# Kernel tuning notes

Measured on AMD Instinct MI355X. Metric: run time of the kernel, lower is better.

The kernel has to match this reference:

```python
import jax, jax.numpy as jnp
import numpy as np

NUM_EXPERTS = 64
HIDDEN = 4096
TOP_K = 2
B, S = 4, 4096


def setup_inputs() -> dict:
    key = jax.random.key(0)
    k1, k2 = jax.random.split(key)
    hidden_states = jax.random.normal(k1, (B, S, HIDDEN), dtype=jnp.float32)
    W = jax.random.normal(k2, (NUM_EXPERTS, HIDDEN), dtype=jnp.float32) * 0.02
    return {"hidden_states": hidden_states, "W": W}


def reference(hidden_states, W):
    # router logits: [B, S, E]
    logits = jnp.einsum("bsh,eh->bse", hidden_states, W)
    flat = logits.reshape(-1, NUM_EXPERTS)  # [T, E]
    # top-k routing (z-loss / aux-loss do not change forward values; they only
    # inject gradients via the custom autograd function in the torch original)
    scores, top_indices = jax.lax.top_k(flat, TOP_K)  # [T, K] each
    return (scores.reshape(B, S, TOP_K), top_indices.reshape(B, S, TOP_K))
```

## Files before the change

kernel.cpp:

```cpp
#include <hip/hip_runtime.h>
#include <hip/hip_bf16.h>
#include <math.h>

#define NUM_EXPERTS 64
#define HIDDEN      4096
#define T_TOKENS    16384

using short8 = __attribute__((ext_vector_type(8))) short;
using f32x4  = __attribute__((ext_vector_type(4))) float;

__device__ __forceinline__ unsigned pack_pair(float f0, float f1, unsigned& lopk) {
    __hip_bfloat162 h2 = __float22bfloat162_rn(make_float2(f0, f1));
    unsigned hb; __builtin_memcpy(&hb, &h2, 4);
    float h0 = __builtin_bit_cast(float, hb << 16);
    float h1 = __builtin_bit_cast(float, hb & 0xffff0000u);
    __hip_bfloat162 l2 = __float22bfloat162_rn(make_float2(f0 - h0, f1 - h1));
    unsigned lb; __builtin_memcpy(&lb, &l2, 4);
    lopk = lb;
    return hb;
}
__device__ __forceinline__ void split8(const float4 a, const float4 b, uint4& hi, uint4& lo) {
    hi.x = pack_pair(a.x, a.y, lo.x);
    hi.y = pack_pair(a.z, a.w, lo.y);
    hi.z = pack_pair(b.x, b.y, lo.z);
    hi.w = pack_pair(b.z, b.w, lo.w);
}

#define MFMA(a, b, c) __builtin_amdgcn_mfma_f32_16x16x32_bf16((a), (b), (c), 0, 0, 0)

#define GLOAD16(g_, l_)                                                        \
    __builtin_amdgcn_global_load_lds(                                          \
        (__attribute__((address_space(1))) unsigned*)(void*)(g_),              \
        (__attribute__((address_space(3))) unsigned*)(void*)(l_), 16, 0, 0)

#define WAITVM(n_)  asm volatile("s_waitcnt vmcnt(" #n_ ")" ::: "memory")
#define WAITLG()    asm volatile("s_waitcnt lgkmcnt(0)" ::: "memory")
#define SB()        __builtin_amdgcn_sched_barrier(0)

__global__ __launch_bounds__(256) void w_split_kernel(
    const float* __restrict__ W, unsigned char* __restrict__ ws)
{
    const int j  = blockIdx.x * 256 + threadIdx.x;
    const int l  = j & 63;
    const int nt = (j >> 6) & 3;
    const int t  = j >> 8;
    const int e  = nt * 16 + (l & 15);
    const int k0 = t * 32 + ((l >> 4) & 3) * 8;
    const float* p = W + (size_t)e * HIDDEN + k0;
    float4 w0 = *reinterpret_cast<const float4*>(p);
    float4 w1 = *reinterpret_cast<const float4*>(p + 4);
    uint4 hi, lo;
    split8(w0, w1, hi, lo);
    *reinterpret_cast<uint4*>(ws + (size_t)j * 16)            = hi;
    *reinterpret_cast<uint4*>(ws + 524288 + (size_t)j * 16)   = lo;
}


#define LOAD_W(dst, t_) do {                                                   \
    const unsigned char* pW_ = wsHi + (size_t)(tBase + (t_)) * 4096 + laneOff; \
    _Pragma("unroll")                                                          \
    for (int nt_ = 0; nt_ < 4; ++nt_) {                                        \
        dst[nt_]     = *reinterpret_cast<const uint4*>(pW_ + nt_ * 1024);      \
        dst[nt_ + 4] = *reinterpret_cast<const uint4*>(pW_ + 524288 + nt_ * 1024); \
    } } while (0)

#define STAGE_A8(b_, t_) do {                                                  \
    unsigned char* ld_ = smem + (size_t)w * 32768 + (b_) * 16384;              \
    const float* g0_ = aBase + (size_t)(t_) * 32;                              \
    _Pragma("unroll")                                                          \
    for (int mt_ = 0; mt_ < 8; ++mt_) {                                        \
        const float* g_ = g0_ + (size_t)mt_ * 16 * HIDDEN;                     \
        GLOAD16(g_,     ld_ + mt_ * 2048);                                     \
        GLOAD16(g_ + 4, ld_ + mt_ * 2048 + 1024);                              \
    } } while (0)

#define SUB_READ(q_, ls_, mt0_) do {                                           \
    _Pragma("unroll")                                                          \
    for (int i_ = 0; i_ < 4; ++i_) {                                           \
        q_[i_][0] = *reinterpret_cast<const float4*>((ls_) + (mt0_ + i_) * 2048);        \
        q_[i_][1] = *reinterpret_cast<const float4*>((ls_) + (mt0_ + i_) * 2048 + 1024); \
    } } while (0)

#define SUB_MFMA(q_, mt0_, wb_) do {                                           \
    _Pragma("unroll")                                                          \
    for (int i_ = 0; i_ < 4; ++i_) {                                           \
        uint4 hi_, lo_;                                                        \
        split8(q_[i_][0], q_[i_][1], hi_, lo_);                                \
        short8 ah_ = __builtin_bit_cast(short8, hi_);                          \
        short8 al_ = __builtin_bit_cast(short8, lo_);                          \
        _Pragma("unroll")                                                      \
        for (int nt_ = 0; nt_ < 4; ++nt_) {                                    \
            short8 wh_ = __builtin_bit_cast(short8, wb_[nt_]);                 \
            short8 wl_ = __builtin_bit_cast(short8, wb_[nt_ + 4]);             \
            acc[mt0_ + i_][nt_] = MFMA(ah_, wh_, acc[mt0_ + i_][nt_]);         \
            acc[mt0_ + i_][nt_] = MFMA(ah_, wl_, acc[mt0_ + i_][nt_]);         \
            acc[mt0_ + i_][nt_] = MFMA(al_, wh_, acc[mt0_ + i_][nt_]);         \
        } } } while (0)

#define ITER_BODY(t_, buf_, wCur_, wNxt_) do {                                 \
    SB();                                                                      \
    const unsigned char* ls_ = smem + (size_t)w * 32768 + (buf_) * 16384 + laneOff; \
    float4 qA_[4][2];                                                          \
    SUB_READ(qA_, ls_, 0);                                                     \
    WAITLG(); SB();                                                            \
    if ((t_) + 1 < 16) LOAD_W(wNxt_, (t_) + 1);                                \
    SUB_MFMA(qA_, 0, wCur_);                                                   \
    float4 qB_[4][2];                                                          \
    SUB_READ(qB_, ls_, 4);                                                     \
    WAITLG(); SB();                                                            \
    if ((t_) + 2 < 16) STAGE_A8(buf_, (t_) + 2);                               \
    SUB_MFMA(qB_, 4, wCur_);                                                   \
} while (0)

#define ITER(t_, buf_, wCur_, wNxt_)      do { WAITVM(16); ITER_BODY(t_, buf_, wCur_, wNxt_); } while (0)
#define ITER_LAST(t_, buf_, wCur_, wNxt_) do { WAITVM(0);  ITER_BODY(t_, buf_, wCur_, wNxt_); } while (0)

__global__ __launch_bounds__(256, 1) void router_gemm_partial(
    const float* __restrict__ A,
    const unsigned char* __restrict__ wsHi,
    float* __restrict__ partG)
{
    __shared__ unsigned char smem[131072];

    const int tid  = threadIdx.x;
    const int lane = tid & 63;
    const int w    = tid >> 6;
    const int ky   = blockIdx.y;
    const int tok0 = blockIdx.x * 128;
    const int tBase = ky * 64 + w * 16;

    const float* aBase = A + (size_t)(tok0 + (lane & 15)) * HIDDEN
                           + ky * 2048 + w * 512 + ((lane >> 4) & 3) * 8;
    const int laneOff = lane * 16;

    f32x4 acc[8][4];
#pragma unroll
    for (int mt = 0; mt < 8; ++mt)
#pragma unroll
        for (int nt = 0; nt < 4; ++nt) acc[mt][nt] = (f32x4){0.f, 0.f, 0.f, 0.f};

    uint4 wX[8], wY[8];

    LOAD_W(wX, 0);
    STAGE_A8(0, 0);
    STAGE_A8(1, 1);

    ITER( 0, 0, wX, wY);  ITER( 1, 1, wY, wX);
    ITER( 2, 0, wX, wY);  ITER( 3, 1, wY, wX);
    ITER( 4, 0, wX, wY);  ITER( 5, 1, wY, wX);
    ITER( 6, 0, wX, wY);  ITER( 7, 1, wY, wX);
    ITER( 8, 0, wX, wY);  ITER( 9, 1, wY, wX);
    ITER(10, 0, wX, wY);  ITER(11, 1, wY, wX);
    ITER(12, 0, wX, wY);  ITER(13, 1, wY, wX);
    ITER(14, 0, wX, wY);  ITER_LAST(15, 1, wY, wX);

    f32x4 (*part)[8][4][64] = reinterpret_cast<f32x4 (*)[8][4][64]>(smem);

    __syncthreads();
#pragma unroll
    for (int mt = 0; mt < 8; ++mt)
#pragma unroll
        for (int nt = 0; nt < 4; ++nt) part[w][mt][nt][lane] = acc[mt][nt];
    __syncthreads();

#pragma unroll
    for (int j = 0; j < 2; ++j) {
        const int mt = 2 * w + j;
#pragma unroll
        for (int nt = 0; nt < 4; ++nt) {
            f32x4 s = part[0][mt][nt][lane];
#pragma unroll
            for (int q = 1; q < 4; ++q) s = s + part[q][mt][nt][lane];
            const int e = nt * 16 + (lane & 15);
#pragma unroll
            for (int r = 0; r < 4; ++r) {
                const int tok = tok0 + mt * 16 + (lane >> 4) * 4 + r;
                partG[((size_t)ky * T_TOKENS + tok) * 64 + e] = s[r];
            }
        }
    }
}

__global__ __launch_bounds__(64) void combine_topk(
    const float* __restrict__ partG,
    float* __restrict__ out)
{
    const int tok = blockIdx.x * 64 + threadIdx.x;
    const float4* p0 = reinterpret_cast<const float4*>(partG + (size_t)tok * 64);
    const float4* p1 = reinterpret_cast<const float4*>(partG + ((size_t)T_TOKENS + tok) * 64);

    float s[64];
#pragma unroll
    for (int i = 0; i < 16; ++i) {
        float4 a = p0[i], b = p1[i];
        s[4*i+0] = a.x + b.x; s[4*i+1] = a.y + b.y;
        s[4*i+2] = a.z + b.z; s[4*i+3] = a.w + b.w;
    }

    float b1 = -INFINITY, b2 = -INFINITY;
    int i1 = 0, i2 = 0;
#pragma unroll
    for (int e = 0; e < NUM_EXPERTS; ++e) {
        float v = s[e];
        if (v > b1)      { b2 = b1; i2 = i1; b1 = v; i1 = e; }
        else if (v > b2) { b2 = v;  i2 = e; }
    }
    out[(size_t)tok * 2 + 0] = b1;
    out[(size_t)tok * 2 + 1] = b2;
    out[(size_t)2 * T_TOKENS + (size_t)tok * 2 + 0] = (float)i1;
    out[(size_t)2 * T_TOKENS + (size_t)tok * 2 + 1] = (float)i2;
}

extern "C" void kernel_launch(void* const* d_in, const int* in_sizes, int n_in,
                              void* d_out, int out_size, void* d_ws, size_t ws_size,
                              hipStream_t stream) {
    const float* A = (const float*)d_in[0];
    const float* W = (const float*)d_in[1];
    float* out = (float*)d_out;
    unsigned char* ws = (unsigned char*)d_ws;
    float* partG = reinterpret_cast<float*>(ws + (1 << 20));

    w_split_kernel<<<dim3(128), dim3(256), 0, stream>>>(W, ws);
    router_gemm_partial<<<dim3(T_TOKENS / 128, 2), dim3(256), 0, stream>>>(A, ws, partG);
    combine_topk<<<dim3(T_TOKENS / 64), dim3(64), 0, stream>>>(partG, out);
}
```

Measured before the change: 61.11 us.

## Split GEMM K-slice across eight waves per block with finer staging

Doubles the router GEMM block to 512 threads (eight waves), each covering half the K range previously assigned per wave, and restructures the A staging into half-size sub-steps with a single-buffer-per-parity LDS layout. Weight fragments are loaded every other sub-step, and the cross-wave reduction gains an extra LDS accumulation pass for the upper four waves. The intent is more resident waves per CU for latency hiding while using the same shared-memory footprint. It adds an extra barrier and reduction traffic, plus launch_bounds(512,2) pressure on registers that could cause spills given the 32 accumulator tiles per wave.

```diff
diff --git a/kernel.cpp b/kernel.cpp
--- a/kernel.cpp
+++ b/kernel.cpp
@@ -64,24 +64,29 @@
         dst[nt_ + 4] = *reinterpret_cast<const uint4*>(pW_ + 524288 + nt_ * 1024); \
     } } while (0)
 
-#define STAGE_A8(b_, t_) do {                                                  \
-    unsigned char* ld_ = smem + (size_t)w * 32768 + (b_) * 16384;              \
-    const float* g0_ = aBase + (size_t)(t_) * 32;                              \
-    _Pragma("unroll")                                                          \
-    for (int mt_ = 0; mt_ < 8; ++mt_) {                                        \
+#define STAGE_S(s_) do {                                                       \
+    unsigned char* ld_ = smem + (size_t)w * 16384 + ((s_) & 1) * 8192;         \
+    const float* g0_ = aBase + (size_t)((s_) >> 1) * 32                        \
+                             + (size_t)(((s_) & 1) * 4) * 16 * HIDDEN;         \
+    _Pragma("unroll")                                                          \
+    for (int mt_ = 0; mt_ < 4; ++mt_) {                                        \
         const float* g_ = g0_ + (size_t)mt_ * 16 * HIDDEN;                     \
         GLOAD16(g_,     ld_ + mt_ * 2048);                                     \
         GLOAD16(g_ + 4, ld_ + mt_ * 2048 + 1024);                              \
     } } while (0)
 
-#define SUB_READ(q_, ls_, mt0_) do {                                           \
+#define SUB_BODY(s_, wCur_, wNxt_) do {                                        \
+    SB();                                                                      \
+    const unsigned char* ls_ = smem + (size_t)w * 16384 + ((s_) & 1) * 8192 + laneOff; \
+    float4 q_[4][2];                                                           \
     _Pragma("unroll")                                                          \
     for (int i_ = 0; i_ < 4; ++i_) {                                           \
-        q_[i_][0] = *reinterpret_cast<const float4*>((ls_) + (mt0_ + i_) * 2048);        \
-        q_[i_][1] = *reinterpret_cast<const float4*>((ls_) + (mt0_ + i_) * 2048 + 1024); \
-    } } while (0)
-
-#define SUB_MFMA(q_, mt0_, wb_) do {                                           \
+        q_[i_][0] = *reinterpret_cast<const float4*>(ls_ + i_ * 2048);         \
+        q_[i_][1] = *reinterpret_cast<const float4*>(ls_ + i_ * 2048 + 1024);  \
+    }                                                                          \
+    WAITLG(); SB();                                                            \
+    if ((((s_) & 1) == 0) && ((s_) / 2 + 1 < 8)) LOAD_W(wNxt_, (s_) / 2 + 1);  \
+    if ((s_) + 2 < 16) STAGE_S((s_) + 2);                                      \
     _Pragma("unroll")                                                          \
     for (int i_ = 0; i_ < 4; ++i_) {                                           \
         uint4 hi_, lo_;                                                        \
@@ -90,32 +95,19 @@
         short8 al_ = __builtin_bit_cast(short8, lo_);                          \
         _Pragma("unroll")                                                      \
         for (int nt_ = 0; nt_ < 4; ++nt_) {                                    \
-            short8 wh_ = __builtin_bit_cast(short8, wb_[nt_]);                 \
-            short8 wl_ = __builtin_bit_cast(short8, wb_[nt_ + 4]);             \
-            acc[mt0_ + i_][nt_] = MFMA(ah_, wh_, acc[mt0_ + i_][nt_]);         \
-            acc[mt0_ + i_][nt_] = MFMA(ah_, wl_, acc[mt0_ + i_][nt_]);         \
-            acc[mt0_ + i_][nt_] = MFMA(al_, wh_, acc[mt0_ + i_][nt_]);         \
-        } } } while (0)
-
-#define ITER_BODY(t_, buf_, wCur_, wNxt_) do {                                 \
-    SB();                                                                      \
-    const unsigned char* ls_ = smem + (size_t)w * 32768 + (buf_) * 16384 + laneOff; \
-    float4 qA_[4][2];                                                          \
-    SUB_READ(qA_, ls_, 0);                                                     \
-    WAITLG(); SB();                                                            \
-    if ((t_) + 1 < 16) LOAD_W(wNxt_, (t_) + 1);                                \
-    SUB_MFMA(qA_, 0, wCur_);                                                   \
-    float4 qB_[4][2];                                                          \
-    SUB_READ(qB_, ls_, 4);                                                     \
-    WAITLG(); SB();                                                            \
-    if ((t_) + 2 < 16) STAGE_A8(buf_, (t_) + 2);                               \
-    SUB_MFMA(qB_, 4, wCur_);                                                   \
+            short8 wh_ = __builtin_bit_cast(short8, wCur_[nt_]);               \
+            short8 wl_ = __builtin_bit_cast(short8, wCur_[nt_ + 4]);           \
+            acc[((s_) & 1) * 4 + i_][nt_] = MFMA(ah_, wh_, acc[((s_) & 1) * 4 + i_][nt_]); \
+            acc[((s_) & 1) * 4 + i_][nt_] = MFMA(ah_, wl_, acc[((s_) & 1) * 4 + i_][nt_]); \
+            acc[((s_) & 1) * 4 + i_][nt_] = MFMA(al_, wh_, acc[((s_) & 1) * 4 + i_][nt_]); \
+        } }                                                                    \
 } while (0)
 
-#define ITER(t_, buf_, wCur_, wNxt_)      do { WAITVM(16); ITER_BODY(t_, buf_, wCur_, wNxt_); } while (0)
-#define ITER_LAST(t_, buf_, wCur_, wNxt_) do { WAITVM(0);  ITER_BODY(t_, buf_, wCur_, wNxt_); } while (0)
-
-__global__ __launch_bounds__(256, 1) void router_gemm_partial(
+#define SUB_E(s_, wC_, wN_) do { WAITVM(8);  SUB_BODY(s_, wC_, wN_); } while (0)
+#define SUB_O(s_, wC_, wN_) do { WAITVM(16); SUB_BODY(s_, wC_, wN_); } while (0)
+#define SUB_Z(s_, wC_, wN_) do { WAITVM(0);  SUB_BODY(s_, wC_, wN_); } while (0)
+
+__global__ __launch_bounds__(512, 2) void router_gemm_partial(
     const float* __restrict__ A,
     const unsigned char* __restrict__ wsHi,
     float* __restrict__ partG)
@@ -127,10 +119,10 @@
     const int w    = tid >> 6;
     const int ky   = blockIdx.y;
     const int tok0 = blockIdx.x * 128;
-    const int tBase = ky * 64 + w * 16;
+    const int tBase = ky * 64 + w * 8;
 
     const float* aBase = A + (size_t)(tok0 + (lane & 15)) * HIDDEN
-                           + ky * 2048 + w * 512 + ((lane >> 4) & 3) * 8;
+                           + ky * 2048 + w * 256 + ((lane >> 4) & 3) * 8;
     const int laneOff = lane * 16;
 
     f32x4 acc[8][4];
@@ -142,40 +134,52 @@
     uint4 wX[8], wY[8];
 
     LOAD_W(wX, 0);
-    STAGE_A8(0, 0);
-    STAGE_A8(1, 1);
-
-    ITER( 0, 0, wX, wY);  ITER( 1, 1, wY, wX);
-    ITER( 2, 0, wX, wY);  ITER( 3, 1, wY, wX);
-    ITER( 4, 0, wX, wY);  ITER( 5, 1, wY, wX);
-    ITER( 6, 0, wX, wY);  ITER( 7, 1, wY, wX);
-    ITER( 8, 0, wX, wY);  ITER( 9, 1, wY, wX);
-    ITER(10, 0, wX, wY);  ITER(11, 1, wY, wX);
-    ITER(12, 0, wX, wY);  ITER(13, 1, wY, wX);
-    ITER(14, 0, wX, wY);  ITER_LAST(15, 1, wY, wX);
+    STAGE_S(0);
+    STAGE_S(1);
+
+    SUB_E( 0, wX, wY);  SUB_O( 1, wX, wY);
+    SUB_E( 2, wY, wX);  SUB_O( 3, wY, wX);
+    SUB_E( 4, wX, wY);  SUB_O( 5, wX, wY);
+    SUB_E( 6, wY, wX);  SUB_O( 7, wY, wX);
+    SUB_E( 8, wX, wY);  SUB_O( 9, wX, wY);
+    SUB_E(10, wY, wX);  SUB_O(11, wY, wX);
+    SUB_E(12, wX, wY);  SUB_O(13, wX, wY);
+    SUB_E(14, wY, wX);  SUB_Z(15, wY, wX);
 
     f32x4 (*part)[8][4][64] = reinterpret_cast<f32x4 (*)[8][4][64]>(smem);
 
     __syncthreads();
-#pragma unroll
-    for (int mt = 0; mt < 8; ++mt)
-#pragma unroll
-        for (int nt = 0; nt < 4; ++nt) part[w][mt][nt][lane] = acc[mt][nt];
+    if (w < 4) {
+#pragma unroll
+        for (int mt = 0; mt < 8; ++mt)
+#pragma unroll
+            for (int nt = 0; nt < 4; ++nt) part[w][mt][nt][lane] = acc[mt][nt];
+    }
     __syncthreads();
-
-#pragma unroll
-    for (int j = 0; j < 2; ++j) {
-        const int mt = 2 * w + j;
-#pragma unroll
-        for (int nt = 0; nt < 4; ++nt) {
-            f32x4 s = part[0][mt][nt][lane];
-#pragma unroll
-            for (int q = 1; q < 4; ++q) s = s + part[q][mt][nt][lane];
-            const int e = nt * 16 + (lane & 15);
-#pragma unroll
-            for (int r = 0; r < 4; ++r) {
-                const int tok = tok0 + mt * 16 + (lane >> 4) * 4 + r;
-                partG[((size_t)ky * T_TOKENS + tok) * 64 + e] = s[r];
+    if (w >= 4) {
+#pragma unroll
+        for (int mt = 0; mt < 8; ++mt)
+#pragma unroll
+            for (int nt = 0; nt < 4; ++nt)
+                part[w - 4][mt][nt][lane] = part[w - 4][mt][nt][lane] + acc[mt][nt];
+    }
+    __syncthreads();
+
+    if (w < 4) {
+#pragma unroll
+        for (int j = 0; j < 2; ++j) {
+            const int mt = 2 * w + j;
+#pragma unroll
+            for (int nt = 0; nt < 4; ++nt) {
+                f32x4 s = part[0][mt][nt][lane];
+#pragma unroll
+                for (int q = 1; q < 4; ++q) s = s + part[q][mt][nt][lane];
+                const int e = nt * 16 + (lane & 15);
+#pragma unroll
+                for (int r = 0; r < 4; ++r) {
+                    const int tok = tok0 + mt * 16 + (lane >> 4) * 4 + r;
+                    partG[((size_t)ky * T_TOKENS + tok) * 64 + e] = s[r];
+                }
             }
         }
     }
@@ -221,6 +225,6 @@
     float* partG = reinterpret_cast<float*>(ws + (1 << 20));
 
     w_split_kernel<<<dim3(128), dim3(256), 0, stream>>>(W, ws);
-    router_gemm_partial<<<dim3(T_TOKENS / 128, 2), dim3(256), 0, stream>>>(A, ws, partG);
+    router_gemm_partial<<<dim3(T_TOKENS / 128, 2), dim3(512), 0, stream>>>(A, ws, partG);
     combine_topk<<<dim3(T_TOKENS / 64), dim3(64), 0, stream>>>(partG, out);
 }
```

After: 77.81 us. +27.3%, slower.
